# Kernel optimization log

Hardware: AMD Instinct MI355X
Metric: run time of the kernel (lower is better)

Reference implementation:

```python
import jax, jax.numpy as jnp
import numpy as np

DIM = 1024
RANK = 16


def setup_inputs() -> dict:
    key = jax.random.key(0)
    ks = jax.random.split(key, 9)
    s = 0.02
    return {
        "x": jax.random.normal(ks[0], (2, 4096, DIM), dtype=jnp.float32),
        "W_qkv": jax.random.normal(ks[1], (3 * DIM, DIM), dtype=jnp.float32) * s,
        "b_qkv": jax.random.normal(ks[2], (3 * DIM,), dtype=jnp.float32) * s,
        "A_q": jax.random.normal(ks[3], (RANK, DIM), dtype=jnp.float32) * s,
        "B_q": jax.random.normal(ks[4], (DIM, RANK), dtype=jnp.float32) * s,
        "A_k": jax.random.normal(ks[5], (RANK, DIM), dtype=jnp.float32) * s,
        "B_k": jax.random.normal(ks[6], (DIM, RANK), dtype=jnp.float32) * s,
        "A_v": jax.random.normal(ks[7], (RANK, DIM), dtype=jnp.float32) * s,
        "B_v": jax.random.normal(ks[8], (DIM, RANK), dtype=jnp.float32) * s,
        "alpha": jnp.float32(0.5),
    }


def reference(x, W_qkv, b_qkv, A_q, B_q, A_k, B_k, A_v, B_v, alpha):
    # base fused QKV projection: [B, S, 3*dim]
    qkv = jnp.einsum("bsd,od->bso", x, W_qkv) + b_qkv
    # low-rank adapters: x @ A.T @ B.T, rank=16
    lora_q = jnp.einsum("bsr,dr->bsd", jnp.einsum("bsd,rd->bsr", x, A_q), B_q)
    lora_k = jnp.einsum("bsr,dr->bsd", jnp.einsum("bsd,rd->bsr", x, A_k), B_k)
    lora_v = jnp.einsum("bsr,dr->bsd", jnp.einsum("bsd,rd->bsr", x, A_v), B_v)
    # scaled add into q/k/v slices (concat order matches torch slice layout)
    delta = jnp.concatenate([lora_q, lora_k, lora_v], axis=-1)
    return qkv + alpha * delta
```

## Files before the change

### kernel.cpp

```cpp
#include <hip/hip_runtime.h>
#include <stdint.h>

#define DIM    1024
#define RANK   16
#define M_TOT  8192
#define N_TOT  3072
#define K_TOT  1024

#define BM 128
#define BN 128
#define BK 64

typedef __attribute__((ext_vector_type(8))) short  s8v;
typedef __attribute__((ext_vector_type(4))) float  f4v;

__device__ __forceinline__ unsigned short f2bf(float f) {
    union { float f; unsigned int u; } v; v.f = f;
    unsigned int u = v.u;
    u += 0x7FFFu + ((u >> 16) & 1u);
    return (unsigned short)(u >> 16);
}

__device__ __forceinline__ void gload_lds16(const unsigned short* g,
                                            unsigned short* l) {
    __builtin_amdgcn_global_load_lds(
        (const __attribute__((address_space(1))) void*)g,
        (__attribute__((address_space(3))) void*)l,
        16, 0, 0);
}

__global__ void prep(const float4* __restrict__ x, ushort4* __restrict__ xb,
                     const float* __restrict__ W,
                     const float* __restrict__ Aq, const float* __restrict__ Bq,
                     const float* __restrict__ Ak, const float* __restrict__ Bk,
                     const float* __restrict__ Av, const float* __restrict__ Bv,
                     const float* __restrict__ alpha_p,
                     unsigned short* __restrict__ Wb) {
    const int tid = threadIdx.x;
    if (blockIdx.x < 8192) {
        int i = blockIdx.x * 256 + tid;
        float4 v = x[i];
        ushort4 o;
        o.x = f2bf(v.x); o.y = f2bf(v.y); o.z = f2bf(v.z); o.w = f2bf(v.w);
        xb[i] = o;
    } else {
        const int o    = blockIdx.x - 8192;
        const int sel  = o >> 10;
        const int orow = o & 1023;
        const float* Am = (sel == 0) ? Aq : (sel == 1) ? Ak : Av;
        const float* Bm = (sel == 0) ? Bq : (sel == 1) ? Bk : Bv;

        __shared__ float sb[RANK];
        if (tid < RANK) sb[tid] = alpha_p[0] * Bm[orow * RANK + tid];
        __syncthreads();

        for (int d = tid; d < DIM; d += 256) {
            float acc = W[o * DIM + d];
            #pragma unroll
            for (int r = 0; r < RANK; ++r)
                acc += sb[r] * Am[r * DIM + d];
            Wb[o * DIM + d] = f2bf(acc);
        }
    }
}

__global__ __launch_bounds__(256, 4)
void gemm_bt(const unsigned short* __restrict__ Xb,
             const unsigned short* __restrict__ Wb,
             const float* __restrict__ bias,
             float* __restrict__ out) {
    __shared__ __align__(16) unsigned short As[BM * BK];
    __shared__ __align__(16) unsigned short Bs[BN * BK];

    const int tid  = threadIdx.x;
    const int wave = tid >> 6;
    const int lane = tid & 63;
    const int l15  = lane & 15;
    const int lq   = lane >> 4;
    const int wr   = wave >> 1;
    const int wc   = wave & 1;

    const int bm = blockIdx.x;
    const int bn = blockIdx.y;

    const unsigned short* aptr[4];
    const unsigned short* bptr[4];
    unsigned short* alds[4];
    unsigned short* blds[4];
    #pragma unroll
    for (int u = 0; u < 4; ++u) {
        const int c   = wave * 4 + u;
        const int row = ((c >> 1) << 4) + l15;
        const int col = ((c & 1) << 5) + (lq << 3);
        aptr[u] = Xb + (size_t)(bm * BM + row) * K_TOT + col;
        bptr[u] = Wb + (size_t)(bn * BN + row) * K_TOT + col;
        alds[u] = &As[c * 512];
        blds[u] = &Bs[c * 512];
    }

    f4v acc[4][4] = {};

    for (int kk = 0; kk < K_TOT; kk += BK) {
        __syncthreads();
        #pragma unroll
        for (int u = 0; u < 4; ++u) {
            gload_lds16(aptr[u] + kk, alds[u]);
            gload_lds16(bptr[u] + kk, blds[u]);
        }
        __syncthreads();

        const s8v* Avp = (const s8v*)As;
        const s8v* Bvp = (const s8v*)Bs;
        #pragma unroll
        for (int t = 0; t < 2; ++t) {
            s8v af[4], bf[4];
            #pragma unroll
            for (int i = 0; i < 4; ++i) {
                const int ia = wr * 4 + i;
                const int jb = wc * 4 + i;
                af[i] = Avp[(ia * 2 + t) * 64 + lane];
                bf[i] = Bvp[(jb * 2 + t) * 64 + lane];
            }
            #pragma unroll
            for (int i = 0; i < 4; ++i)
                #pragma unroll
                for (int j = 0; j < 4; ++j)
                    acc[i][j] = __builtin_amdgcn_mfma_f32_16x16x32_bf16(
                        af[i], bf[j], acc[i][j], 0, 0, 0);
        }
    }

    const int col_base = bn * BN + wc * 64;
    const int row_base = bm * BM + wr * 64 + lq * 4;
    #pragma unroll
    for (int j = 0; j < 4; ++j) {
        const int col = col_base + j * 16 + l15;
        const float bv = bias[col];
        #pragma unroll
        for (int i = 0; i < 4; ++i) {
            const int row = row_base + i * 16;
            #pragma unroll
            for (int r = 0; r < 4; ++r)
                out[(size_t)(row + r) * N_TOT + col] = acc[i][j][r] + bv;
        }
    }
}

extern "C" void kernel_launch(void* const* d_in, const int* in_sizes, int n_in,
                              void* d_out, int out_size, void* d_ws, size_t ws_size,
                              hipStream_t stream) {
    const float* x     = (const float*)d_in[0];
    const float* W     = (const float*)d_in[1];
    const float* b     = (const float*)d_in[2];
    const float* Aq    = (const float*)d_in[3];
    const float* Bq    = (const float*)d_in[4];
    const float* Ak    = (const float*)d_in[5];
    const float* Bk    = (const float*)d_in[6];
    const float* Av    = (const float*)d_in[7];
    const float* Bv    = (const float*)d_in[8];
    const float* alpha = (const float*)d_in[9];
    float* out = (float*)d_out;

    unsigned short* xb = (unsigned short*)d_ws;
    unsigned short* Wb = (unsigned short*)((char*)d_ws + (size_t)M_TOT * K_TOT * 2);

    prep<<<8192 + N_TOT, 256, 0, stream>>>((const float4*)x, (ushort4*)xb,
                                           W, Aq, Bq, Ak, Bk, Av, Bv, alpha, Wb);

    dim3 grid(M_TOT / BM, N_TOT / BN);
    gemm_bt<<<grid, 256, 0, stream>>>(xb, Wb, b, out);
}
```

Baseline: 271.1 us.

## Double-buffer LDS tiles with async prefetch, enlarge M tile, remap blocks per XCD

Doubles the M tile to 256 rows with 512-thread blocks and allocates two LDS buffers for A and B. Global-to-LDS loads for tile k+2 are issued right after compute on tile k, with explicit vmcnt waits and barriers, so memory latency overlaps MFMA work. Workgroup IDs are remapped so blocks interleaved across XCDs share B columns, which should improve L2 reuse. The cost is more LDS per block (96 KB) and lower occupancy, and correctness now depends on the hand-counted vmcnt values.

Result: faster. 261.0 us (-3.7%).

```diff
diff --git a/kernel.cpp b/kernel.cpp
--- a/kernel.cpp
+++ b/kernel.cpp
@@ -7,9 +7,10 @@
 #define N_TOT  3072
 #define K_TOT  1024
 
-#define BM 128
+#define BM 256
 #define BN 128
 #define BK 64
+#define NT (K_TOT / BK)
 
 typedef __attribute__((ext_vector_type(8))) short  s8v;
 typedef __attribute__((ext_vector_type(4))) float  f4v;
@@ -64,13 +65,13 @@
     }
 }
 
-__global__ __launch_bounds__(256, 4)
+__global__ __launch_bounds__(512, 2)
 void gemm_bt(const unsigned short* __restrict__ Xb,
              const unsigned short* __restrict__ Wb,
              const float* __restrict__ bias,
              float* __restrict__ out) {
-    __shared__ __align__(16) unsigned short As[BM * BK];
-    __shared__ __align__(16) unsigned short Bs[BN * BK];
+    __shared__ __align__(16) unsigned short As[2][BM * BK];
+    __shared__ __align__(16) unsigned short Bs[2][BN * BK];
 
     const int tid  = threadIdx.x;
     const int wave = tid >> 6;
@@ -80,46 +81,60 @@
     const int wr   = wave >> 1;
     const int wc   = wave & 1;
 
-    const int bm = blockIdx.x;
-    const int bn = blockIdx.y;
+    const int bid  = blockIdx.x;
+    const int wgid = (bid & 7) * 96 + (bid >> 3);
+    const int bn   = wgid >> 5;
+    const int bm   = wgid & 31;
 
     const unsigned short* aptr[4];
-    const unsigned short* bptr[4];
-    unsigned short* alds[4];
-    unsigned short* blds[4];
+    const unsigned short* bptr[2];
+    int aoff[4], boff[2];
     #pragma unroll
     for (int u = 0; u < 4; ++u) {
         const int c   = wave * 4 + u;
         const int row = ((c >> 1) << 4) + l15;
         const int col = ((c & 1) << 5) + (lq << 3);
         aptr[u] = Xb + (size_t)(bm * BM + row) * K_TOT + col;
+        aoff[u] = c * 512;
+    }
+    #pragma unroll
+    for (int u = 0; u < 2; ++u) {
+        const int c   = wave * 2 + u;
+        const int row = ((c >> 1) << 4) + l15;
+        const int col = ((c & 1) << 5) + (lq << 3);
         bptr[u] = Wb + (size_t)(bn * BN + row) * K_TOT + col;
-        alds[u] = &As[c * 512];
-        blds[u] = &Bs[c * 512];
+        boff[u] = c * 512;
+    }
+
+    #pragma unroll
+    for (int t = 0; t < 2; ++t) {
+        #pragma unroll
+        for (int u = 0; u < 4; ++u) gload_lds16(aptr[u] + t * BK, &As[t][aoff[u]]);
+        #pragma unroll
+        for (int u = 0; u < 2; ++u) gload_lds16(bptr[u] + t * BK, &Bs[t][boff[u]]);
     }
 
     f4v acc[4][4] = {};
 
-    for (int kk = 0; kk < K_TOT; kk += BK) {
-        __syncthreads();
-        #pragma unroll
-        for (int u = 0; u < 4; ++u) {
-            gload_lds16(aptr[u] + kk, alds[u]);
-            gload_lds16(bptr[u] + kk, blds[u]);
-        }
-        __syncthreads();
-
-        const s8v* Avp = (const s8v*)As;
-        const s8v* Bvp = (const s8v*)Bs;
+    #pragma unroll
+    for (int kt = 0; kt < NT; ++kt) {
+        const int cur = kt & 1;
+        if (kt < NT - 1) asm volatile("s_waitcnt vmcnt(6)" ::: "memory");
+        else             asm volatile("s_waitcnt vmcnt(0)" ::: "memory");
+        __builtin_amdgcn_sched_barrier(0);
+        __builtin_amdgcn_s_barrier();
+        __builtin_amdgcn_sched_barrier(0);
+        asm volatile("" ::: "memory");
+
+        const s8v* Avp = (const s8v*)As[cur];
+        const s8v* Bvp = (const s8v*)Bs[cur];
         #pragma unroll
         for (int t = 0; t < 2; ++t) {
             s8v af[4], bf[4];
             #pragma unroll
             for (int i = 0; i < 4; ++i) {
-                const int ia = wr * 4 + i;
-                const int jb = wc * 4 + i;
-                af[i] = Avp[(ia * 2 + t) * 64 + lane];
-                bf[i] = Bvp[(jb * 2 + t) * 64 + lane];
+                af[i] = Avp[((wr * 4 + i) * 2 + t) * 64 + lane];
+                bf[i] = Bvp[((wc * 4 + i) * 2 + t) * 64 + lane];
             }
             #pragma unroll
             for (int i = 0; i < 4; ++i)
@@ -127,6 +142,20 @@
                 for (int j = 0; j < 4; ++j)
                     acc[i][j] = __builtin_amdgcn_mfma_f32_16x16x32_bf16(
                         af[i], bf[j], acc[i][j], 0, 0, 0);
+        }
+
+        asm volatile("" ::: "memory");
+        __builtin_amdgcn_sched_barrier(0);
+        __builtin_amdgcn_s_barrier();
+        __builtin_amdgcn_sched_barrier(0);
+
+        if (kt < NT - 2) {
+            #pragma unroll
+            for (int u = 0; u < 4; ++u)
+                gload_lds16(aptr[u] + (kt + 2) * BK, &As[cur][aoff[u]]);
+            #pragma unroll
+            for (int u = 0; u < 2; ++u)
+                gload_lds16(bptr[u] + (kt + 2) * BK, &Bs[cur][boff[u]]);
         }
     }
 
@@ -167,6 +196,5 @@
     prep<<<8192 + N_TOT, 256, 0, stream>>>((const float4*)x, (ushort4*)xb,
                                            W, Aq, Bq, Ak, Bk, Av, Bv, alpha, Wb);
 
-    dim3 grid(M_TOT / BM, N_TOT / BN);
-    gemm_bt<<<grid, 256, 0, stream>>>(xb, Wb, b, out);
-}
+    gemm_bt<<<(M_TOT / BM) * (N_TOT / BN), 512, 0, stream>>>(xb, Wb, b, out);
+}
```
